# Optimization experiments

Hardware: AMD Instinct MI355X
Metric: run time of the kernel (lower is better)

## Reference

```python
import jax, jax.numpy as jnp
import numpy as np

B, S, H, E = 4096, 200, 128, 64


def setup_inputs() -> dict:
    key = jax.random.key(0)
    ks = jax.random.split(key, 10)
    s = 0.05  # small init scale for weight matrices
    return {
        "interest_states": jax.random.normal(ks[0], (B, S, H), jnp.float32),
        "target_item": jax.random.normal(ks[1], (B, E), jnp.float32),
        "W_bil": jax.random.normal(ks[2], (H, E), jnp.float32) * s,
        "Wxu": jax.random.normal(ks[3], (H, H), jnp.float32) * s,
        "Whu": jax.random.normal(ks[4], (H, H), jnp.float32) * s,
        "bu": jnp.zeros((H,), jnp.float32),
        "Wxr": jax.random.normal(ks[5], (H, H), jnp.float32) * s,
        "Whr": jax.random.normal(ks[6], (H, H), jnp.float32) * s,
        "br": jnp.zeros((H,), jnp.float32),
        "Wxc": jax.random.normal(ks[7], (H, H), jnp.float32) * s,
        "Whc": jax.random.normal(ks[8], (H, H), jnp.float32) * s,
        "bc": jnp.zeros((H,), jnp.float32),
    }


def reference(interest_states, target_item, W_bil, Wxu, Whu, bu, Wxr, Whr, br, Wxc, Whc, bc):
    # Bilinear attention: a_t = softmax_t(h_t W e_a)  -> [B, S]
    logits = jnp.einsum('bsh,he,be->bs', interest_states, W_bil, target_item)
    att = jax.nn.softmax(logits, axis=1)

    def step(h, xs):
        x, a = xs  # x: [B, H], a: [B]
        u = jax.nn.sigmoid(x @ Wxu + h @ Whu + bu)          # update gate
        r = jax.nn.sigmoid(x @ Wxr + h @ Whr + br)          # reset gate
        c = jnp.tanh(x @ Wxc + (r * h) @ Whc + bc)          # candidate
        au = a[:, None] * u                                  # attention-scaled update gate
        h_new = (1.0 - au) * h + au * c
        return h_new, None

    h0 = jnp.zeros((interest_states.shape[0], Wxu.shape[1]), interest_states.dtype)
    xs = (jnp.swapaxes(interest_states, 0, 1), att.T)  # time-major: [S,B,H], [S,B]
    h_final, _ = jax.lax.scan(step, h0, xs)
    return h_final  # [B, H]
```

## Files before the change

kernel.cpp:

```cpp
#include <hip/hip_runtime.h>

typedef __attribute__((ext_vector_type(8))) short short8;
typedef __attribute__((ext_vector_type(4))) short short4v;
typedef __attribute__((ext_vector_type(4))) float float4v;

#define Hh 128
#define Ss 200
#define Ee 64
#define BR 16
#define TPB3 512

#if defined(__has_builtin) && __has_builtin(__builtin_amdgcn_exp2f)
#define EXP2F(x) __builtin_amdgcn_exp2f(x)
#else
#define EXP2F(x) exp2f(x)
#endif
#if defined(__has_builtin) && __has_builtin(__builtin_amdgcn_rcpf)
#define RCPF(x) __builtin_amdgcn_rcpf(x)
#else
#define RCPF(x) (1.0f / (x))
#endif

#define LOG2E 1.442695040888963f

__device__ __forceinline__ float fsig(float z) {
    return RCPF(1.0f + EXP2F(-LOG2E * z));
}
__device__ __forceinline__ float ftanh(float z) {
    return 1.0f - 2.0f * RCPF(1.0f + EXP2F(2.0f * LOG2E * z));
}

__device__ __forceinline__ short f2bf(float f) {
    unsigned u = __float_as_uint(f);
    u += 0x7FFFu + ((u >> 16) & 1u);
    return (short)(u >> 16);
}
__device__ __forceinline__ float bf2f(short s) {
    return __uint_as_float(((unsigned)(unsigned short)s) << 16);
}

__global__ __launch_bounds__(TPB3) void fused_kernel(
    const float* __restrict__ x, const float* __restrict__ tgt,
    const float* __restrict__ Wb,
    const float* __restrict__ Wxu, const float* __restrict__ Whu, const float* __restrict__ bu,
    const float* __restrict__ Wxr, const float* __restrict__ Whr, const float* __restrict__ br,
    const float* __restrict__ Wxc, const float* __restrict__ Whc, const float* __restrict__ bc,
    float* __restrict__ out)
{
    __shared__ __align__(16) short xh[BR][264];
    __shared__ __align__(16) short rhs[BR][136];
    __shared__ __align__(16) float G1[BR][132];
    __shared__ __align__(16) float C2[BR][132];
    __shared__ float attS[BR][Ss];

    int tid = threadIdx.x;
    int wave = tid >> 6, lane = tid & 63;
    int quad = lane >> 4, l16 = lane & 15;
    int b0 = blockIdx.x * BR;

    float* tg = &C2[0][0];
    float* vv = &G1[0][0];

    for (int i = tid; i < BR * Ee; i += TPB3) tg[i] = tgt[(size_t)b0 * Ee + i];
    __syncthreads();

    {
        int h = tid & 127, rq = tid >> 7;
        float acc[4] = {0.f, 0.f, 0.f, 0.f};
        const float* wr = Wb + (size_t)h * Ee;
        #pragma unroll
        for (int e4 = 0; e4 < Ee / 4; ++e4) {
            float4v wv = *(const float4v*)&wr[e4 * 4];
            #pragma unroll
            for (int ro = 0; ro < 4; ++ro) {
                float4v tv = *(const float4v*)&tg[(rq * 4 + ro) * Ee + e4 * 4];
                acc[ro] += wv.x * tv.x + wv.y * tv.y + wv.z * tv.z + wv.w * tv.w;
            }
        }
        #pragma unroll
        for (int ro = 0; ro < 4; ++ro) vv[(rq * 4 + ro) * Hh + h] = acc[ro];
    }
    __syncthreads();

    #pragma unroll 1
    for (int rr = 0; rr < 2; ++rr) {
        int r = wave * 2 + rr;
        float vr[8];
        *(float4v*)&vr[0] = *(const float4v*)&vv[r * Hh + l16 * 8];
        *(float4v*)&vr[4] = *(const float4v*)&vv[r * Hh + l16 * 8 + 4];
        const float* xb = x + ((size_t)(b0 + r) * Ss) * Hh + l16 * 8;
        for (int s0 = quad * 4; s0 < Ss; s0 += 16) {
            float4v xa[4][2];
            #pragma unroll
            for (int j = 0; j < 4; ++j) {
                const float* xr = xb + (size_t)(s0 + j) * Hh;
                xa[j][0] = *(const float4v*)xr;
                xa[j][1] = *(const float4v*)(xr + 4);
            }
            #pragma unroll
            for (int j = 0; j < 4; ++j) {
                float d = xa[j][0].x * vr[0] + xa[j][0].y * vr[1]
                        + xa[j][0].z * vr[2] + xa[j][0].w * vr[3]
                        + xa[j][1].x * vr[4] + xa[j][1].y * vr[5]
                        + xa[j][1].z * vr[6] + xa[j][1].w * vr[7];
                d += __shfl_xor(d, 8);
                d += __shfl_xor(d, 4);
                d += __shfl_xor(d, 2);
                d += __shfl_xor(d, 1);
                if (l16 == 0) attS[r][s0 + j] = d;
            }
        }
    }
    #pragma unroll 1
    for (int rr = 0; rr < 2; ++rr) {
        int r = wave * 2 + rr;
        float vals[4], m = -1e30f;
        #pragma unroll
        for (int i = 0; i < 4; ++i) {
            int s = lane + i * 64;
            vals[i] = (s < Ss) ? attS[r][s] : -1e30f;
            m = fmaxf(m, vals[i]);
        }
        #pragma unroll
        for (int off = 32; off > 0; off >>= 1) m = fmaxf(m, __shfl_xor(m, off));
        float z = 0.f;
        #pragma unroll
        for (int i = 0; i < 4; ++i) {
            int s = lane + i * 64;
            vals[i] = (s < Ss) ? EXP2F((vals[i] - m) * LOG2E) : 0.f;
            z += vals[i];
        }
        #pragma unroll
        for (int off = 32; off > 0; off >>= 1) z += __shfl_xor(z, off);
        float zi = RCPF(z);
        #pragma unroll
        for (int i = 0; i < 4; ++i) {
            int s = lane + i * 64;
            if (s < Ss) attS[r][s] = vals[i] * zi;
        }
    }
    __syncthreads();

    short8 W1[2][8];
    short8 W2[8];
    #pragma unroll
    for (int t = 0; t < 2; ++t) {
        int fullcol = wave * 32 + t * 16 + l16;
        const float* Wx = (fullcol < 128) ? Wxu : Wxr;
        const float* Wh = (fullcol < 128) ? Whu : Whr;
        int n = fullcol & 127;
        #pragma unroll
        for (int q = 0; q < 8; ++q) {
            short8 f;
            #pragma unroll
            for (int j = 0; j < 8; ++j) {
                int k = q * 32 + quad * 8 + j;
                float wv = (k < 128) ? Wx[k * Hh + n] : Wh[(k - 128) * Hh + n];
                f[j] = f2bf(wv);
            }
            W1[t][q] = f;
        }
    }
    {
        int n2 = wave * 16 + l16;
        #pragma unroll
        for (int q = 0; q < 8; ++q) {
            short8 f;
            #pragma unroll
            for (int j = 0; j < 8; ++j) {
                int k = q * 32 + quad * 8 + j;
                float wv = (k < 128) ? Wxc[k * Hh + n2] : Whc[(k - 128) * Hh + n2];
                f[j] = f2bf(wv);
            }
            W2[q] = f;
        }
    }
    float b1[2];
    #pragma unroll
    for (int t = 0; t < 2; ++t) {
        int fullcol = wave * 32 + t * 16 + l16;
        b1[t] = (fullcol < 128) ? bu[fullcol] : br[fullcol - 128];
    }
    float b2 = bc[wave * 16 + l16];

    int urow = tid >> 5;
    int uc = (tid & 31) * 4;
    float hreg[4] = {0.f, 0.f, 0.f, 0.f};
    { short4v z = {0, 0, 0, 0}; *(short4v*)&xh[urow][128 + uc] = z; }

    const float* xrow = x + (size_t)(b0 + urow) * Ss * Hh + uc;
    float4v xv = *(const float4v*)&xrow[0];
    float4v xvn = xv;

    #pragma unroll 1
    for (int t = 0; t < Ss; ++t) {
        {
            short4v xs;
            #pragma unroll
            for (int i = 0; i < 4; ++i) xs[i] = f2bf(xv[i]);
            *(short4v*)&xh[urow][uc] = xs;
        }
        if (t + 1 < Ss) xvn = *(const float4v*)&xrow[(size_t)(t + 1) * Hh];
        __syncthreads();

        float4v a0 = {0.f, 0.f, 0.f, 0.f}, a1 = {0.f, 0.f, 0.f, 0.f};
        #pragma unroll
        for (int q = 0; q < 8; ++q) {
            short8 af = *(const short8*)&xh[l16][q * 32 + quad * 8];
            a0 = __builtin_amdgcn_mfma_f32_16x16x32_bf16(af, W1[0][q], a0, 0, 0, 0);
            a1 = __builtin_amdgcn_mfma_f32_16x16x32_bf16(af, W1[1][q], a1, 0, 0, 0);
        }
        if (wave < 4) {
            int c0 = wave * 32 + l16;
            #pragma unroll
            for (int r = 0; r < 4; ++r) {
                int rr = quad * 4 + r;
                G1[rr][c0]      = fsig(a0[r] + b1[0]);
                G1[rr][c0 + 16] = fsig(a1[r] + b1[1]);
            }
        } else {
            int c0 = (wave - 4) * 32 + l16;
            #pragma unroll
            for (int r = 0; r < 4; ++r) {
                int rr = quad * 4 + r;
                float r0 = fsig(a0[r] + b1[0]);
                float r1 = fsig(a1[r] + b1[1]);
                float h0 = bf2f(xh[rr][128 + c0]);
                float h1 = bf2f(xh[rr][128 + c0 + 16]);
                rhs[rr][c0]      = f2bf(r0 * h0);
                rhs[rr][c0 + 16] = f2bf(r1 * h1);
            }
        }
        __syncthreads();

        float4v a2 = {0.f, 0.f, 0.f, 0.f};
        #pragma unroll
        for (int q = 0; q < 4; ++q) {
            short8 af = *(const short8*)&xh[l16][q * 32 + quad * 8];
            a2 = __builtin_amdgcn_mfma_f32_16x16x32_bf16(af, W2[q], a2, 0, 0, 0);
        }
        #pragma unroll
        for (int q = 0; q < 4; ++q) {
            short8 af = *(const short8*)&rhs[l16][q * 32 + quad * 8];
            a2 = __builtin_amdgcn_mfma_f32_16x16x32_bf16(af, W2[q + 4], a2, 0, 0, 0);
        }
        {
            int c0 = wave * 16 + l16;
            #pragma unroll
            for (int r = 0; r < 4; ++r)
                C2[quad * 4 + r][c0] = ftanh(a2[r] + b2);
        }
        __syncthreads();

        {
            float a = attS[urow][t];
            short4v hv;
            #pragma unroll
            for (int i = 0; i < 4; ++i) {
                float u = G1[urow][uc + i];
                float c = C2[urow][uc + i];
                float au = a * u;
                hreg[i] = (1.f - au) * hreg[i] + au * c;
                hv[i] = f2bf(hreg[i]);
            }
            *(short4v*)&xh[urow][128 + uc] = hv;
        }
        xv = xvn;
    }

    float4v o;
    #pragma unroll
    for (int i = 0; i < 4; ++i) o[i] = hreg[i];
    *(float4v*)&out[(size_t)(b0 + urow) * Hh + uc] = o;
}

extern "C" void kernel_launch(void* const* d_in, const int* in_sizes, int n_in,
                              void* d_out, int out_size, void* d_ws, size_t ws_size,
                              hipStream_t stream) {
    const float* x   = (const float*)d_in[0];
    const float* tgt = (const float*)d_in[1];
    const float* Wb  = (const float*)d_in[2];
    const float* Wxu = (const float*)d_in[3];
    const float* Whu = (const float*)d_in[4];
    const float* bu  = (const float*)d_in[5];
    const float* Wxr = (const float*)d_in[6];
    const float* Whr = (const float*)d_in[7];
    const float* br  = (const float*)d_in[8];
    const float* Wxc = (const float*)d_in[9];
    const float* Whc = (const float*)d_in[10];
    const float* bc  = (const float*)d_in[11];
    float* out = (float*)d_out;

    const int B = in_sizes[1] / Ee;

    fused_kernel<<<B / BR, TPB3, 0, stream>>>(x, tgt, Wb, Wxu, Whu, bu,
                                              Wxr, Whr, br, Wxc, Whc, bc, out);
}
```

Measured before the change: 833.6 us.

## Keep GRU gates and hidden state in MFMA registers, drop a barrier per step

Each wave now owns the same 16 output columns for the update, reset and candidate gates, so u, r*h and the hidden-state update can be computed directly from MFMA accumulators in registers instead of going through G1/C2 shared buffers. This removes one __syncthreads per timestep and the extra LDS round-trips. The x tile is double-buffered so the next step's input can be written during the current one, and attention is transposed so a float4 read serves a quad. The trade-offs are more weight registers per thread (three 8-fragment sets) and a scalar, non-vectorized final output store.

```diff
diff --git a/kernel.cpp b/kernel.cpp
--- a/kernel.cpp
+++ b/kernel.cpp
@@ -35,9 +35,6 @@
     u += 0x7FFFu + ((u >> 16) & 1u);
     return (short)(u >> 16);
 }
-__device__ __forceinline__ float bf2f(short s) {
-    return __uint_as_float(((unsigned)(unsigned short)s) << 16);
-}
 
 __global__ __launch_bounds__(TPB3) void fused_kernel(
     const float* __restrict__ x, const float* __restrict__ tgt,
@@ -47,19 +44,18 @@
     const float* __restrict__ Wxc, const float* __restrict__ Whc, const float* __restrict__ bc,
     float* __restrict__ out)
 {
-    __shared__ __align__(16) short xh[BR][264];
+    __shared__ __align__(16) short xarr[2][BR][136];
+    __shared__ __align__(16) short harr[BR][136];
     __shared__ __align__(16) short rhs[BR][136];
-    __shared__ __align__(16) float G1[BR][132];
-    __shared__ __align__(16) float C2[BR][132];
-    __shared__ float attS[BR][Ss];
+    __shared__ __align__(16) float attS[Ss][BR];
 
     int tid = threadIdx.x;
     int wave = tid >> 6, lane = tid & 63;
     int quad = lane >> 4, l16 = lane & 15;
     int b0 = blockIdx.x * BR;
 
-    float* tg = &C2[0][0];
-    float* vv = &G1[0][0];
+    float* vv = (float*)&xarr[0][0][0];
+    float* tg = (float*)&rhs[0][0];
 
     for (int i = tid; i < BR * Ee; i += TPB3) tg[i] = tgt[(size_t)b0 * Ee + i];
     __syncthreads();
@@ -107,7 +103,7 @@
                 d += __shfl_xor(d, 4);
                 d += __shfl_xor(d, 2);
                 d += __shfl_xor(d, 1);
-                if (l16 == 0) attS[r][s0 + j] = d;
+                if (l16 == 0) attS[s0 + j][r] = d;
             }
         }
     }
@@ -118,7 +114,7 @@
         #pragma unroll
         for (int i = 0; i < 4; ++i) {
             int s = lane + i * 64;
-            vals[i] = (s < Ss) ? attS[r][s] : -1e30f;
+            vals[i] = (s < Ss) ? attS[s][r] : -1e30f;
             m = fmaxf(m, vals[i]);
         }
         #pragma unroll
@@ -136,142 +132,107 @@
         #pragma unroll
         for (int i = 0; i < 4; ++i) {
             int s = lane + i * 64;
-            if (s < Ss) attS[r][s] = vals[i] * zi;
+            if (s < Ss) attS[s][r] = vals[i] * zi;
         }
     }
     __syncthreads();
 
-    short8 W1[2][8];
-    short8 W2[8];
+    int col = wave * 16 + l16;
+    short8 W1u[8], W1r[8], W2[8];
     #pragma unroll
-    for (int t = 0; t < 2; ++t) {
-        int fullcol = wave * 32 + t * 16 + l16;
-        const float* Wx = (fullcol < 128) ? Wxu : Wxr;
-        const float* Wh = (fullcol < 128) ? Whu : Whr;
-        int n = fullcol & 127;
-        #pragma unroll
-        for (int q = 0; q < 8; ++q) {
-            short8 f;
-            #pragma unroll
-            for (int j = 0; j < 8; ++j) {
-                int k = q * 32 + quad * 8 + j;
-                float wv = (k < 128) ? Wx[k * Hh + n] : Wh[(k - 128) * Hh + n];
-                f[j] = f2bf(wv);
-            }
-            W1[t][q] = f;
-        }
-    }
+    for (int q = 0; q < 8; ++q) {
+        short8 fu, fr, fc;
+        #pragma unroll
+        for (int j = 0; j < 8; ++j) {
+            int k = q * 32 + quad * 8 + j;
+            float wu = (k < 128) ? Wxu[k * Hh + col] : Whu[(k - 128) * Hh + col];
+            float wr_ = (k < 128) ? Wxr[k * Hh + col] : Whr[(k - 128) * Hh + col];
+            float wc = (k < 128) ? Wxc[k * Hh + col] : Whc[(k - 128) * Hh + col];
+            fu[j] = f2bf(wu);
+            fr[j] = f2bf(wr_);
+            fc[j] = f2bf(wc);
+        }
+        W1u[q] = fu; W1r[q] = fr; W2[q] = fc;
+    }
+    float b1u = bu[col], b1r = br[col], b2v = bc[col];
+
+    int srow = tid >> 5, scol = (tid & 31) * 4;
+    const float* xrow = x + (size_t)(b0 + srow) * Ss * Hh + scol;
+    float4v xv = *(const float4v*)xrow;
     {
-        int n2 = wave * 16 + l16;
-        #pragma unroll
-        for (int q = 0; q < 8; ++q) {
-            short8 f;
-            #pragma unroll
-            for (int j = 0; j < 8; ++j) {
-                int k = q * 32 + quad * 8 + j;
-                float wv = (k < 128) ? Wxc[k * Hh + n2] : Whc[(k - 128) * Hh + n2];
-                f[j] = f2bf(wv);
-            }
-            W2[q] = f;
-        }
-    }
-    float b1[2];
+        short4v xs;
+        #pragma unroll
+        for (int i = 0; i < 4; ++i) xs[i] = f2bf(xv[i]);
+        *(short4v*)&xarr[0][srow][scol] = xs;
+    }
+    float hreg[4] = {0.f, 0.f, 0.f, 0.f};
     #pragma unroll
-    for (int t = 0; t < 2; ++t) {
-        int fullcol = wave * 32 + t * 16 + l16;
-        b1[t] = (fullcol < 128) ? bu[fullcol] : br[fullcol - 128];
-    }
-    float b2 = bc[wave * 16 + l16];
-
-    int urow = tid >> 5;
-    int uc = (tid & 31) * 4;
-    float hreg[4] = {0.f, 0.f, 0.f, 0.f};
-    { short4v z = {0, 0, 0, 0}; *(short4v*)&xh[urow][128 + uc] = z; }
-
-    const float* xrow = x + (size_t)(b0 + urow) * Ss * Hh + uc;
-    float4v xv = *(const float4v*)&xrow[0];
-    float4v xvn = xv;
+    for (int r = 0; r < 4; ++r) harr[quad * 4 + r][col] = 0;
+
+    float4v xv1 = xv;
 
     #pragma unroll 1
     for (int t = 0; t < Ss; ++t) {
+        __syncthreads();
+        int par = t & 1;
+
+        if (t + 1 < Ss) xv1 = *(const float4v*)&xrow[(size_t)(t + 1) * Hh];
+
+        float4v a0a = {0.f,0.f,0.f,0.f}, a0b = {0.f,0.f,0.f,0.f};
+        float4v a1a = {0.f,0.f,0.f,0.f}, a1b = {0.f,0.f,0.f,0.f};
+        #pragma unroll
+        for (int q = 0; q < 4; ++q) {
+            short8 af = *(const short8*)&xarr[par][l16][q * 32 + quad * 8];
+            a0a = __builtin_amdgcn_mfma_f32_16x16x32_bf16(af, W1u[q], a0a, 0, 0, 0);
+            a1a = __builtin_amdgcn_mfma_f32_16x16x32_bf16(af, W1r[q], a1a, 0, 0, 0);
+        }
+        #pragma unroll
+        for (int q = 0; q < 4; ++q) {
+            short8 af = *(const short8*)&harr[l16][q * 32 + quad * 8];
+            a0b = __builtin_amdgcn_mfma_f32_16x16x32_bf16(af, W1u[q + 4], a0b, 0, 0, 0);
+            a1b = __builtin_amdgcn_mfma_f32_16x16x32_bf16(af, W1r[q + 4], a1b, 0, 0, 0);
+        }
+        float ureg[4];
+        #pragma unroll
+        for (int r = 0; r < 4; ++r) {
+            ureg[r] = fsig(a0a[r] + a0b[r] + b1u);
+            float rg = fsig(a1a[r] + a1b[r] + b1r);
+            rhs[quad * 4 + r][col] = f2bf(rg * hreg[r]);
+        }
+        __syncthreads();
+
+        float4v a2a = {0.f,0.f,0.f,0.f}, a2b = {0.f,0.f,0.f,0.f};
+        #pragma unroll
+        for (int q = 0; q < 4; ++q) {
+            short8 af = *(const short8*)&xarr[par][l16][q * 32 + quad * 8];
+            a2a = __builtin_amdgcn_mfma_f32_16x16x32_bf16(af, W2[q], a2a, 0, 0, 0);
+        }
+        #pragma unroll
+        for (int q = 0; q < 4; ++q) {
+            short8 af = *(const short8*)&rhs[l16][q * 32 + quad * 8];
+            a2b = __builtin_amdgcn_mfma_f32_16x16x32_bf16(af, W2[q + 4], a2b, 0, 0, 0);
+        }
         {
+            float4v av = *(const float4v*)&attS[t][quad * 4];
+            #pragma unroll
+            for (int r = 0; r < 4; ++r) {
+                float c = ftanh(a2a[r] + a2b[r] + b2v);
+                float au = av[r] * ureg[r];
+                hreg[r] = (1.f - au) * hreg[r] + au * c;
+                harr[quad * 4 + r][col] = f2bf(hreg[r]);
+            }
+        }
+        if (t + 1 < Ss) {
             short4v xs;
             #pragma unroll
-            for (int i = 0; i < 4; ++i) xs[i] = f2bf(xv[i]);
-            *(short4v*)&xh[urow][uc] = xs;
-        }
-        if (t + 1 < Ss) xvn = *(const float4v*)&xrow[(size_t)(t + 1) * Hh];
-        __syncthreads();
-
-        float4v a0 = {0.f, 0.f, 0.f, 0.f}, a1 = {0.f, 0.f, 0.f, 0.f};
-        #pragma unroll
-        for (int q = 0; q < 8; ++q) {
-            short8 af = *(const short8*)&xh[l16][q * 32 + quad * 8];
-            a0 = __builtin_amdgcn_mfma_f32_16x16x32_bf16(af, W1[0][q], a0, 0, 0, 0);
-            a1 = __builtin_amdgcn_mfma_f32_16x16x32_bf16(af, W1[1][q], a1, 0, 0, 0);
-        }
-        if (wave < 4) {
-            int c0 = wave * 32 + l16;
-            #pragma unroll
-            for (int r = 0; r < 4; ++r) {
-                int rr = quad * 4 + r;
-                G1[rr][c0]      = fsig(a0[r] + b1[0]);
-                G1[rr][c0 + 16] = fsig(a1[r] + b1[1]);
-            }
-        } else {
-            int c0 = (wave - 4) * 32 + l16;
-            #pragma unroll
-            for (int r = 0; r < 4; ++r) {
-                int rr = quad * 4 + r;
-                float r0 = fsig(a0[r] + b1[0]);
-                float r1 = fsig(a1[r] + b1[1]);
-                float h0 = bf2f(xh[rr][128 + c0]);
-                float h1 = bf2f(xh[rr][128 + c0 + 16]);
-                rhs[rr][c0]      = f2bf(r0 * h0);
-                rhs[rr][c0 + 16] = f2bf(r1 * h1);
-            }
-        }
-        __syncthreads();
-
-        float4v a2 = {0.f, 0.f, 0.f, 0.f};
-        #pragma unroll
-        for (int q = 0; q < 4; ++q) {
-            short8 af = *(const short8*)&xh[l16][q * 32 + quad * 8];
-            a2 = __builtin_amdgcn_mfma_f32_16x16x32_bf16(af, W2[q], a2, 0, 0, 0);
-        }
-        #pragma unroll
-        for (int q = 0; q < 4; ++q) {
-            short8 af = *(const short8*)&rhs[l16][q * 32 + quad * 8];
-            a2 = __builtin_amdgcn_mfma_f32_16x16x32_bf16(af, W2[q + 4], a2, 0, 0, 0);
-        }
-        {
-            int c0 = wave * 16 + l16;
-            #pragma unroll
-            for (int r = 0; r < 4; ++r)
-                C2[quad * 4 + r][c0] = ftanh(a2[r] + b2);
-        }
-        __syncthreads();
-
-        {
-            float a = attS[urow][t];
-            short4v hv;
-            #pragma unroll
-            for (int i = 0; i < 4; ++i) {
-                float u = G1[urow][uc + i];
-                float c = C2[urow][uc + i];
-                float au = a * u;
-                hreg[i] = (1.f - au) * hreg[i] + au * c;
-                hv[i] = f2bf(hreg[i]);
-            }
-            *(short4v*)&xh[urow][128 + uc] = hv;
-        }
-        xv = xvn;
-    }
-
-    float4v o;
+            for (int i = 0; i < 4; ++i) xs[i] = f2bf(xv1[i]);
+            *(short4v*)&xarr[par ^ 1][srow][scol] = xs;
+        }
+    }
+
     #pragma unroll
-    for (int i = 0; i < 4; ++i) o[i] = hreg[i];
-    *(float4v*)&out[(size_t)(b0 + urow) * Hh + uc] = o;
+    for (int r = 0; r < 4; ++r)
+        out[(size_t)(b0 + quad * 4 + r) * Hh + col] = hreg[r];
 }
 
 extern "C" void kernel_launch(void* const* d_in, const int* in_sizes, int n_in,
```

Result: faster. 790.2 us (-5.2%).
